# Optimization experiments

Hardware: AMD Instinct MI355X
Metric: run time of the kernel (lower is better)

The kernel has to match this reference:

```python
import jax, jax.numpy as jnp
import numpy as np

B, S, D, H, F = 4, 2048, 1024, 16, 4096
BS = 64               # sparse attention block size
DH = D // H           # head dim
EPS = 1e-5


def _layer_norm(x, g, b):
    m = jnp.mean(x, axis=-1, keepdims=True)
    v = jnp.mean(jnp.square(x - m), axis=-1, keepdims=True)
    return (x - m) * jax.lax.rsqrt(v + EPS) * g + b


def setup_inputs() -> dict:
    key = jax.random.key(0)
    ks = jax.random.split(key, 12)
    sc = 0.02
    return {
        "hidden_states": jax.random.normal(ks[0], (B, S, D), dtype=jnp.float32),
        "ln1_g": jnp.ones((D,), jnp.float32), "ln1_b": jnp.zeros((D,), jnp.float32),
        "ln2_g": jnp.ones((D,), jnp.float32), "ln2_b": jnp.zeros((D,), jnp.float32),
        "wq": jax.random.normal(ks[1], (D, D), jnp.float32) * sc, "bq": jnp.zeros((D,), jnp.float32),
        "wk": jax.random.normal(ks[2], (D, D), jnp.float32) * sc, "bk": jnp.zeros((D,), jnp.float32),
        "wv": jax.random.normal(ks[3], (D, D), jnp.float32) * sc, "bv": jnp.zeros((D,), jnp.float32),
        "wo": jax.random.normal(ks[4], (D, D), jnp.float32) * sc, "bo": jnp.zeros((D,), jnp.float32),
        "w1": jax.random.normal(ks[5], (D, F), jnp.float32) * sc, "b1": jnp.zeros((F,), jnp.float32),
        "w2": jax.random.normal(ks[6], (F, D), jnp.float32) * sc, "b2": jnp.zeros((D,), jnp.float32),
    }


def _heads(x, w, b):
    # [B,S,D] -> [B,H,S/BS,BS,DH] block layout
    y = (x @ w + b).reshape(B, S, H, DH).transpose(0, 2, 1, 3)
    return y.reshape(B, H, S // BS, BS, DH)


def _block_attention(x, wq, bq, wk, bk, wv, bv, wo, bo):
    q = _heads(x, wq, bq)
    k = _heads(x, wk, bk)
    v = _heads(x, wv, bv)
    scores = jnp.einsum("bhnqd,bhnkd->bhnqk", q, k) / jnp.sqrt(jnp.float32(DH))
    w = jax.nn.softmax(scores, axis=-1)           # block-local (sparse) attention weights
    o = jnp.einsum("bhnqk,bhnkd->bhnqd", w, v)
    o = o.reshape(B, H, S, DH).transpose(0, 2, 1, 3).reshape(B, S, D)
    return o @ wo + bo, w


def reference(hidden_states, ln1_g, ln1_b, ln2_g, ln2_b,
              wq, bq, wk, bk, wv, bv, wo, bo, w1, b1, w2, b2):
    # pre-norm attention + residual
    x1 = _layer_norm(hidden_states, ln1_g, ln1_b)
    attn_out, attn_w = _block_attention(x1, wq, bq, wk, bk, wv, bv, wo, bo)
    h = hidden_states + attn_out
    # pre-norm FFN + residual (exact GELU, matching torch nn.GELU default)
    x2 = _layer_norm(h, ln2_g, ln2_b)
    ff = jax.nn.gelu(x2 @ w1 + b1, approximate=False) @ w2 + b2
    return h + ff, attn_w
```

## Files before the change

### kernel.cpp

```cpp
#include <hip/hip_runtime.h>
#include <hip/hip_bf16.h>
#include <cmath>
#include <type_traits>

using bf16 = __hip_bfloat16;
typedef __attribute__((ext_vector_type(8))) short short8;
typedef __attribute__((ext_vector_type(4))) float f32x4;

#define LDK 72

__device__ __forceinline__ float bf2f(bf16 v){ return __bfloat162float(v); }
__device__ __forceinline__ bf16 f2bf(float v){ return __float2bfloat16(v); }

__device__ __forceinline__ void ld16(const void* g, void* l) {
    __builtin_amdgcn_global_load_lds(
        (const __attribute__((address_space(1))) void*)g,
        (__attribute__((address_space(3))) void*)l, 16, 0, 0);
}

__device__ __forceinline__ float gelu_f(float x) {
    float u = 0.7978845608028654f * x * (1.0f + 0.044715f * x * x);
    float e = __expf(2.0f * u);
    float t = 1.0f - 2.0f / (e + 1.0f);
    return 0.5f * x * (1.0f + t);
}

__global__ __launch_bounds__(256) void transpose_f32_bf16(
    const float* __restrict__ in, bf16* __restrict__ out, int R, int C)
{
    __shared__ __align__(16) bf16 tile[64][72];
    const int c0 = blockIdx.x * 64, r0 = blockIdx.y * 64;
    const int t = threadIdx.x;
    const int lr = t >> 3, lc = (t & 7) * 8;
    for (int p = 0; p < 2; ++p) {
        int r = p * 32 + lr;
        const float* src = in + (size_t)(r0 + r) * C + c0 + lc;
        float4 a = *(const float4*)src;
        float4 b = *(const float4*)(src + 4);
        tile[r][lc + 0] = f2bf(a.x); tile[r][lc + 1] = f2bf(a.y);
        tile[r][lc + 2] = f2bf(a.z); tile[r][lc + 3] = f2bf(a.w);
        tile[r][lc + 4] = f2bf(b.x); tile[r][lc + 5] = f2bf(b.y);
        tile[r][lc + 6] = f2bf(b.z); tile[r][lc + 7] = f2bf(b.w);
    }
    __syncthreads();
    for (int p = 0; p < 2; ++p) {
        int r = p * 32 + lr;
        short8 v;
        for (int j = 0; j < 8; ++j) v[j] = *(const short*)&tile[lc + j][r];
        *(short8*)(out + (size_t)(c0 + r) * R + r0 + lc) = v;
    }
}

__global__ __launch_bounds__(256) void concat_bias(
    const float* __restrict__ bq, const float* __restrict__ bk,
    const float* __restrict__ bv, float* __restrict__ out)
{
    int i = blockIdx.x * 256 + threadIdx.x;
    const float* src = (i < 1024) ? bq : ((i < 2048) ? bk : bv);
    out[i] = src[i & 1023];
}

__global__ __launch_bounds__(256) void layernorm_k(
    const float* __restrict__ x, const float* __restrict__ g,
    const float* __restrict__ bta, bf16* __restrict__ out)
{
    const int row = blockIdx.x, t = threadIdx.x;
    const float* xr = x + (size_t)row * 1024;
    float v[4], s1 = 0.f, s2 = 0.f;
    for (int j = 0; j < 4; ++j) {
        float f = xr[j * 256 + t];
        v[j] = f; s1 += f; s2 += f * f;
    }
    for (int d = 1; d < 64; d <<= 1) { s1 += __shfl_xor(s1, d); s2 += __shfl_xor(s2, d); }
    __shared__ float red[2][4];
    int wave = t >> 6, lane = t & 63;
    if (lane == 0) { red[0][wave] = s1; red[1][wave] = s2; }
    __syncthreads();
    s1 = red[0][0] + red[0][1] + red[0][2] + red[0][3];
    s2 = red[1][0] + red[1][1] + red[1][2] + red[1][3];
    float mean = s1 * (1.0f / 1024.0f);
    float var  = s2 * (1.0f / 1024.0f) - mean * mean;
    float rs   = rsqrtf(var + 1e-5f);
    bf16* orow = out + (size_t)row * 1024;
    for (int j = 0; j < 4; ++j) {
        int c = j * 256 + t;
        orow[c] = f2bf((v[j] - mean) * rs * g[c] + bta[c]);
    }
}

template <int MODE, int KT>
__global__ __launch_bounds__(512, 1) void gemm256(
    const bf16* __restrict__ A, const bf16* __restrict__ Bt,
    const float* __restrict__ bias, void* __restrict__ C,
    int M, int N)
{
    __shared__ __align__(16) bf16 smem[2][2][256 * 64];
    const int m0 = blockIdx.x * 256, n0 = blockIdx.y * 256;
    const int t = threadIdx.x;
    const int wave = t >> 6, lane = t & 63, lhi = lane >> 4, llo = lane & 15;
    const int wm = (wave >> 2) * 128;
    const int wn = (wave & 3) * 64;
    const int lrow = lane >> 3, lcol = lane & 7;
    const int gsrc = (lcol ^ lrow) * 8;

    const int axb = (wave >> 2) * 128 + (wave & 3) * 8;
    const int bxb = (wave & 3) * 64 + (wave >> 2) * 16;

    const bf16* gAX0 = A  + (size_t)(m0 + lrow + axb) * KT + gsrc;
    const bf16* gAX1 = gAX0 + (size_t)32 * KT;
    const bf16* gAY0 = gAX0 + (size_t)64 * KT;
    const bf16* gAY1 = gAX0 + (size_t)96 * KT;
    const bf16* gBX0 = Bt + (size_t)(n0 + lrow + bxb) * KT + gsrc;
    const bf16* gBX1 = gBX0 + (size_t)8 * KT;
    const bf16* gBY0 = gBX0 + (size_t)32 * KT;
    const bf16* gBY1 = gBX0 + (size_t)40 * KT;

    const int swz   = llo & 7;
    const int offA0 = (wm + llo) * 64 + ((lhi ^ swz) * 8);
    const int offA1 = (wm + llo) * 64 + ((((4 + lhi)) ^ swz) * 8);
    const int offB0 = (wn + llo) * 64 + ((lhi ^ swz) * 8);
    const int offB1 = (wn + llo) * 64 + ((((4 + lhi)) ^ swz) * 8);

    f32x4 acc[8][4];
    #pragma unroll
    for (int i = 0; i < 8; ++i)
        #pragma unroll
        for (int j = 0; j < 4; ++j) acc[i][j] = (f32x4){0.f, 0.f, 0.f, 0.f};

    constexpr int T = KT / 64;
    static_assert(T % 2 == 0, "tail assumes even tile count");

#define SBR __builtin_amdgcn_sched_barrier(0)

    ld16(gAX0, &smem[0][0][axb * 64]);        ld16(gAX1, &smem[0][0][(axb + 32) * 64]);
    ld16(gBX0, &smem[0][1][bxb * 64]);        ld16(gBX1, &smem[0][1][(bxb + 8) * 64]);
    ld16(gAY0, &smem[0][0][(axb + 64) * 64]); ld16(gAY1, &smem[0][0][(axb + 96) * 64]);
    ld16(gBY0, &smem[0][1][(bxb + 32) * 64]); ld16(gBY1, &smem[0][1][(bxb + 40) * 64]);
    gAX0 += 64; gAX1 += 64; gAY0 += 64; gAY1 += 64;
    gBX0 += 64; gBX1 += 64; gBY0 += 64; gBY1 += 64;

    auto tile = [&](auto cbc) __attribute__((always_inline)) {
        constexpr int CB = decltype(cbc)::value;
        constexpr int NB = CB ^ 1;
        short8 aX[4][2], bX[2][2], aY[4][2], bY[2][2];
        ld16(gAX0, &smem[NB][0][axb * 64]);
        ld16(gAX1, &smem[NB][0][(axb + 32) * 64]);
        asm volatile("s_waitcnt vmcnt(6)" ::: "memory");
        SBR; __builtin_amdgcn_s_barrier(); SBR;
        #pragma unroll
        for (int mi = 0; mi < 4; ++mi) {
            aX[mi][0] = *(const short8*)&smem[CB][0][offA0 + mi * 1024];
            aX[mi][1] = *(const short8*)&smem[CB][0][offA1 + mi * 1024];
        }
        #pragma unroll
        for (int ni = 0; ni < 2; ++ni) {
            bX[ni][0] = *(const short8*)&smem[CB][1][offB0 + ni * 1024];
            bX[ni][1] = *(const short8*)&smem[CB][1][offB1 + ni * 1024];
        }
        __builtin_amdgcn_s_setprio(1);
        #pragma unroll
        for (int mi = 0; mi < 4; ++mi)
            #pragma unroll
            for (int ni = 0; ni < 2; ++ni)
                #pragma unroll
                for (int kk = 0; kk < 2; ++kk)
                    acc[mi][ni] = __builtin_amdgcn_mfma_f32_16x16x32_bf16(
                        aX[mi][kk], bX[ni][kk], acc[mi][ni], 0, 0, 0);
        __builtin_amdgcn_s_setprio(0);
        ld16(gBX0, &smem[NB][1][bxb * 64]);
        ld16(gBX1, &smem[NB][1][(bxb + 8) * 64]);
        asm volatile("s_waitcnt vmcnt(4)" ::: "memory");
        SBR; __builtin_amdgcn_s_barrier(); SBR;
        #pragma unroll
        for (int ni = 0; ni < 2; ++ni) {
            bY[ni][0] = *(const short8*)&smem[CB][1][offB0 + (ni + 2) * 1024];
            bY[ni][1] = *(const short8*)&smem[CB][1][offB1 + (ni + 2) * 1024];
        }
        __builtin_amdgcn_s_setprio(1);
        #pragma unroll
        for (int mi = 0; mi < 4; ++mi)
            #pragma unroll
            for (int ni = 0; ni < 2; ++ni)
                #pragma unroll
                for (int kk = 0; kk < 2; ++kk)
                    acc[mi][ni + 2] = __builtin_amdgcn_mfma_f32_16x16x32_bf16(
                        aX[mi][kk], bY[ni][kk], acc[mi][ni + 2], 0, 0, 0);
        __builtin_amdgcn_s_setprio(0);
        ld16(gAY0, &smem[NB][0][(axb + 64) * 64]);
        ld16(gAY1, &smem[NB][0][(axb + 96) * 64]);
        #pragma unroll
        for (int mi = 0; mi < 4; ++mi) {
            aY[mi][0] = *(const short8*)&smem[CB][0][offA0 + (mi + 4) * 1024];
            aY[mi][1] = *(const short8*)&smem[CB][0][offA1 + (mi + 4) * 1024];
        }
        __builtin_amdgcn_s_setprio(1);
        #pragma unroll
        for (int mi = 0; mi < 4; ++mi)
            #pragma unroll
            for (int ni = 0; ni < 2; ++ni)
                #pragma unroll
                for (int kk = 0; kk < 2; ++kk)
                    acc[mi + 4][ni] = __builtin_amdgcn_mfma_f32_16x16x32_bf16(
                        aY[mi][kk], bX[ni][kk], acc[mi + 4][ni], 0, 0, 0);
        __builtin_amdgcn_s_setprio(0);
        ld16(gBY0, &smem[NB][1][(bxb + 32) * 64]);
        ld16(gBY1, &smem[NB][1][(bxb + 40) * 64]);
        asm volatile("s_waitcnt lgkmcnt(0)" ::: "memory");
        SBR; __builtin_amdgcn_s_barrier(); SBR;
        __builtin_amdgcn_s_setprio(1);
        #pragma unroll
        for (int mi = 0; mi < 4; ++mi)
            #pragma unroll
            for (int ni = 0; ni < 2; ++ni)
                #pragma unroll
                for (int kk = 0; kk < 2; ++kk)
                    acc[mi + 4][ni + 2] = __builtin_amdgcn_mfma_f32_16x16x32_bf16(
                        aY[mi][kk], bY[ni][kk], acc[mi + 4][ni + 2], 0, 0, 0);
        __builtin_amdgcn_s_setprio(0);
        gAX0 += 64; gAX1 += 64; gAY0 += 64; gAY1 += 64;
        gBX0 += 64; gBX1 += 64; gBY0 += 64; gBY1 += 64;
    };

    for (int jp = 0; jp < (T - 2) / 2; ++jp) {
        tile(std::integral_constant<int, 0>{});
        tile(std::integral_constant<int, 1>{});
    }
    tile(std::integral_constant<int, 0>{});

    {
        short8 aX[4][2], bX[2][2], aY[4][2], bY[2][2];
        asm volatile("s_waitcnt vmcnt(4)" ::: "memory");
        SBR; __builtin_amdgcn_s_barrier(); SBR;
        #pragma unroll
        for (int mi = 0; mi < 4; ++mi) {
            aX[mi][0] = *(const short8*)&smem[1][0][offA0 + mi * 1024];
            aX[mi][1] = *(const short8*)&smem[1][0][offA1 + mi * 1024];
        }
        #pragma unroll
        for (int ni = 0; ni < 2; ++ni) {
            bX[ni][0] = *(const short8*)&smem[1][1][offB0 + ni * 1024];
            bX[ni][1] = *(const short8*)&smem[1][1][offB1 + ni * 1024];
        }
        __builtin_amdgcn_s_setprio(1);
        #pragma unroll
        for (int mi = 0; mi < 4; ++mi)
            #pragma unroll
            for (int ni = 0; ni < 2; ++ni)
                #pragma unroll
                for (int kk = 0; kk < 2; ++kk)
                    acc[mi][ni] = __builtin_amdgcn_mfma_f32_16x16x32_bf16(
                        aX[mi][kk], bX[ni][kk], acc[mi][ni], 0, 0, 0);
        __builtin_amdgcn_s_setprio(0);
        asm volatile("s_waitcnt vmcnt(0)" ::: "memory");
        SBR; __builtin_amdgcn_s_barrier(); SBR;
        #pragma unroll
        for (int ni = 0; ni < 2; ++ni) {
            bY[ni][0] = *(const short8*)&smem[1][1][offB0 + (ni + 2) * 1024];
            bY[ni][1] = *(const short8*)&smem[1][1][offB1 + (ni + 2) * 1024];
        }
        #pragma unroll
        for (int mi = 0; mi < 4; ++mi) {
            aY[mi][0] = *(const short8*)&smem[1][0][offA0 + (mi + 4) * 1024];
            aY[mi][1] = *(const short8*)&smem[1][0][offA1 + (mi + 4) * 1024];
        }
        __builtin_amdgcn_s_setprio(1);
        #pragma unroll
        for (int mi = 0; mi < 4; ++mi)
            #pragma unroll
            for (int ni = 0; ni < 2; ++ni)
                #pragma unroll
                for (int kk = 0; kk < 2; ++kk) {
                    acc[mi][ni + 2] = __builtin_amdgcn_mfma_f32_16x16x32_bf16(
                        aX[mi][kk], bY[ni][kk], acc[mi][ni + 2], 0, 0, 0);
                    acc[mi + 4][ni] = __builtin_amdgcn_mfma_f32_16x16x32_bf16(
                        aY[mi][kk], bX[ni][kk], acc[mi + 4][ni], 0, 0, 0);
                    acc[mi + 4][ni + 2] = __builtin_amdgcn_mfma_f32_16x16x32_bf16(
                        aY[mi][kk], bY[ni][kk], acc[mi + 4][ni + 2], 0, 0, 0);
                }
        __builtin_amdgcn_s_setprio(0);
    }
#undef SBR

    #pragma unroll
    for (int mi = 0; mi < 8; ++mi)
        #pragma unroll
        for (int ni = 0; ni < 4; ++ni) {
            int row = m0 + wm + mi * 16 + lhi * 4;
            int col = n0 + wn + ni * 16 + llo;
            float bcol = bias[col];
            #pragma unroll
            for (int r = 0; r < 4; ++r) {
                size_t idx = (size_t)(row + r) * N + col;
                float v = acc[mi][ni][r] + bcol;
                if (MODE == 2) ((bf16*)C)[idx] = f2bf(gelu_f(v));
                else           ((bf16*)C)[idx] = f2bf(v);
            }
        }
}

template <int MODE, int TM>
__global__ __launch_bounds__(256) void gemm_bt(
    const bf16* __restrict__ A, const bf16* __restrict__ Bt,
    const float* __restrict__ bias, const float* __restrict__ res,
    void* __restrict__ C, int M, int N, int K)
{
    constexpr int MI = TM / 32;
    __shared__ __align__(16) bf16 As[TM * 64];
    __shared__ __align__(16) bf16 Bs[128 * 64];
    const int m0 = blockIdx.x * TM, n0 = blockIdx.y * 128;
    const int t = threadIdx.x;
    const int wave = t >> 6, lane = t & 63, lhi = lane >> 4, llo = lane & 15;
    const int wm = (wave & 1) * (TM / 2), wn = (wave >> 1) * 64;
    const int lrow = lane >> 3;
    const int lcolsw = ((lane & 7) ^ lrow) * 8;

    const bf16* Ag = A  + (size_t)(m0 + lrow) * K + lcolsw;
    const bf16* Bg = Bt + (size_t)(n0 + lrow) * K + lcolsw;

    f32x4 acc[MI][4];
    for (int i = 0; i < MI; ++i)
        for (int j = 0; j < 4; ++j) acc[i][j] = (f32x4){0.f, 0.f, 0.f, 0.f};

    auto issue = [&](int k0) {
        for (int p = 0; p < TM / 32; ++p) {
            int rb = wave * (TM / 4) + p * 8;
            ld16(Ag + (size_t)rb * K + k0, &As[rb * 64]);
        }
        for (int p = 0; p < 4; ++p) {
            int rb = wave * 32 + p * 8;
            ld16(Bg + (size_t)rb * K + k0, &Bs[rb * 64]);
        }
    };
    auto compute = [&]() {
        for (int kk = 0; kk < 64; kk += 32) {
            const int gb = kk >> 3;
            short8 af[MI], bfr[4];
            for (int i = 0; i < MI; ++i) {
                int row = wm + i * 16 + llo;
                af[i] = *(const short8*)&As[row * 64 + (((gb + lhi) ^ (llo & 7)) * 8)];
            }
            for (int i = 0; i < 4; ++i) {
                int row = wn + i * 16 + llo;
                bfr[i] = *(const short8*)&Bs[row * 64 + (((gb + lhi) ^ (llo & 7)) * 8)];
            }
            for (int mi = 0; mi < MI; ++mi)
                for (int ni = 0; ni < 4; ++ni)
                    acc[mi][ni] = __builtin_amdgcn_mfma_f32_16x16x32_bf16(
                        af[mi], bfr[ni], acc[mi][ni], 0, 0, 0);
        }
    };

    issue(0);
    __syncthreads();
    for (int k0 = 0; ; ) {
        compute();
        k0 += 64;
        if (k0 >= K) break;
        __syncthreads();
        issue(k0);
        __syncthreads();
    }

    for (int mi = 0; mi < MI; ++mi)
        for (int ni = 0; ni < 4; ++ni) {
            int row = m0 + wm + mi * 16 + lhi * 4;
            int col = n0 + wn + ni * 16 + llo;
            float bcol = bias[col];
            for (int r = 0; r < 4; ++r) {
                size_t idx = (size_t)(row + r) * N + col;
                float v = acc[mi][ni][r] + bcol;
                if (MODE == 0) {
                    ((bf16*)C)[idx] = f2bf(v);
                } else if (MODE == 1) {
                    ((float*)C)[idx] = v + res[idx];
                } else if (MODE == 2) {
                    ((bf16*)C)[idx] = f2bf(gelu_f(v));
                } else {
                    ((float*)C)[idx] = v + res[idx];
                }
            }
        }
}

__global__ __launch_bounds__(256) void attn_kernel(
    const bf16* __restrict__ qkv, float* __restrict__ attw, bf16* __restrict__ o)
{
    __shared__ __align__(16) bf16 qs[64][LDK];
    __shared__ __align__(16) bf16 ks[64][LDK];
    __shared__ __align__(16) bf16 vs[64][LDK];
    const int gid = blockIdx.x;
    const int blk = gid & 31, h = (gid >> 5) & 15, b = gid >> 9;
    const int t = threadIdx.x, wave = t >> 6, lane = t & 63;
    const int lhi = lane >> 4, llo = lane & 15;
    const int srow = t >> 3, scol = (t & 7) * 8;

    for (int p = 0; p < 2; ++p) {
        int r = p * 32 + srow;
        const bf16* base = qkv + (size_t)(b * 2048 + blk * 64 + r) * 3072 + h * 64 + scol;
        *(short8*)&qs[r][scol] = *(const short8*)(base);
        *(short8*)&ks[r][scol] = *(const short8*)(base + 1024);
        *(short8*)&vs[r][scol] = *(const short8*)(base + 2048);
    }
    __syncthreads();

    f32x4 sacc[4];
    for (int j = 0; j < 4; ++j) sacc[j] = (f32x4){0.f, 0.f, 0.f, 0.f};
    for (int kk = 0; kk < 64; kk += 32) {
        short8 aq = *(const short8*)&qs[wave * 16 + llo][kk + lhi * 8];
        for (int j = 0; j < 4; ++j) {
            short8 bk = *(const short8*)&ks[j * 16 + llo][kk + lhi * 8];
            sacc[j] = __builtin_amdgcn_mfma_f32_16x16x32_bf16(aq, bk, sacc[j], 0, 0, 0);
        }
    }
    float inv[4];
    for (int r = 0; r < 4; ++r) {
        float m = -1e30f;
        for (int j = 0; j < 4; ++j) m = fmaxf(m, sacc[j][r]);
        for (int d = 1; d < 16; d <<= 1) m = fmaxf(m, __shfl_xor(m, d));
        float s = 0.f;
        for (int j = 0; j < 4; ++j) {
            float e = expf((sacc[j][r] - m) * 0.125f);
            sacc[j][r] = e; s += e;
        }
        for (int d = 1; d < 16; d <<= 1) s += __shfl_xor(s, d);
        inv[r] = 1.0f / s;
    }
    __syncthreads();
    const size_t wbase = (size_t)gid * 4096;
    for (int j = 0; j < 4; ++j)
        for (int r = 0; r < 4; ++r) {
            int row = wave * 16 + lhi * 4 + r, col = j * 16 + llo;
            float pw = sacc[j][r] * inv[r];
            qs[row][col] = f2bf(pw);
            attw[wbase + row * 64 + col] = pw;
        }
    __syncthreads();

    f32x4 oacc[4];
    for (int nt = 0; nt < 4; ++nt) oacc[nt] = (f32x4){0.f, 0.f, 0.f, 0.f};
    for (int kk = 0; kk < 64; kk += 32) {
        short8 aw = *(const short8*)&qs[wave * 16 + llo][kk + lhi * 8];
        for (int nt = 0; nt < 4; ++nt) {
            short8 bv;
            for (int jj = 0; jj < 8; ++jj)
                bv[jj] = *(const short*)&vs[kk + lhi * 8 + jj][nt * 16 + llo];
            oacc[nt] = __builtin_amdgcn_mfma_f32_16x16x32_bf16(aw, bv, oacc[nt], 0, 0, 0);
        }
    }
    for (int nt = 0; nt < 4; ++nt)
        for (int r = 0; r < 4; ++r) {
            int row = wave * 16 + lhi * 4 + r, col = nt * 16 + llo;
            o[(size_t)(b * 2048 + blk * 64 + row) * 1024 + h * 64 + col] = f2bf(oacc[nt][r]);
        }
}

extern "C" void kernel_launch(void* const* d_in, const int* in_sizes, int n_in,
                              void* d_out, int out_size, void* d_ws, size_t ws_size,
                              hipStream_t stream)
{
    const float* hidden = (const float*)d_in[0];
    const float* ln1_g  = (const float*)d_in[1];
    const float* ln1_b  = (const float*)d_in[2];
    const float* ln2_g  = (const float*)d_in[3];
    const float* ln2_b  = (const float*)d_in[4];
    const float* wq = (const float*)d_in[5];  const float* bq = (const float*)d_in[6];
    const float* wk = (const float*)d_in[7];  const float* bk = (const float*)d_in[8];
    const float* wv = (const float*)d_in[9];  const float* bv = (const float*)d_in[10];
    const float* wo = (const float*)d_in[11]; const float* bo = (const float*)d_in[12];
    const float* w1 = (const float*)d_in[13]; const float* b1 = (const float*)d_in[14];
    const float* w2 = (const float*)d_in[15]; const float* b2 = (const float*)d_in[16];

    char* ws = (char*)d_ws;
    const size_t MB = 1u << 20;
    bf16*  wqkvT   = (bf16*)(ws +  0 * MB);
    bf16*  woT     = (bf16*)(ws +  6 * MB);
    bf16*  w1T     = (bf16*)(ws +  8 * MB);
    bf16*  w2T     = (bf16*)(ws + 16 * MB);
    float* biasQKV = (float*)(ws + 24 * MB);
    bf16*  x       = (bf16*)(ws + 25 * MB);
    bf16*  qkv     = (bf16*)(ws + 41 * MB);
    float* hbuf    = (float*)(ws + 41 * MB);
    bf16*  ffc     = (bf16*)(ws + 73 * MB);
    bf16*  obuf    = (bf16*)(ws + 89 * MB);

    float* out0 = (float*)d_out;
    float* attw = (float*)d_out + (size_t)8192 * 1024;

    transpose_f32_bf16<<<dim3(16, 16), 256, 0, stream>>>(wq, wqkvT,                 1024, 1024);
    transpose_f32_bf16<<<dim3(16, 16), 256, 0, stream>>>(wk, wqkvT + 1024 * 1024,   1024, 1024);
    transpose_f32_bf16<<<dim3(16, 16), 256, 0, stream>>>(wv, wqkvT + 2*1024*1024,   1024, 1024);
    transpose_f32_bf16<<<dim3(16, 16), 256, 0, stream>>>(wo, woT, 1024, 1024);
    transpose_f32_bf16<<<dim3(64, 16), 256, 0, stream>>>(w1, w1T, 1024, 4096);
    transpose_f32_bf16<<<dim3(16, 64), 256, 0, stream>>>(w2, w2T, 4096, 1024);
    concat_bias<<<12, 256, 0, stream>>>(bq, bk, bv, biasQKV);

    layernorm_k<<<8192, 256, 0, stream>>>(hidden, ln1_g, ln1_b, x);

    gemm256<0, 1024><<<dim3(32, 12), 512, 0, stream>>>(x, wqkvT, biasQKV, qkv,
                                                       8192, 3072);

    attn_kernel<<<2048, 256, 0, stream>>>(qkv, attw, obuf);

    gemm_bt<1, 128><<<dim3(64, 8), 256, 0, stream>>>(obuf, woT, bo, hidden, hbuf,
                                                     8192, 1024, 1024);

    layernorm_k<<<8192, 256, 0, stream>>>(hbuf, ln2_g, ln2_b, x);

    gemm256<2, 1024><<<dim3(32, 16), 512, 0, stream>>>(x, w1T, b1, ffc,
                                                       8192, 4096);

    gemm_bt<3, 128><<<dim3(64, 8), 256, 0, stream>>>(ffc, w2T, b2, hbuf, out0,
                                                     8192, 1024, 4096);
}
```

Measured before the change: 418.6 us.

## Merge weight transposes into one launch and rework GEMM barrier schedule

```diff
diff --git a/kernel.cpp b/kernel.cpp
--- a/kernel.cpp
+++ b/kernel.cpp
@@ -25,11 +25,34 @@
     return 0.5f * x * (1.0f + t);
 }
 
-__global__ __launch_bounds__(256) void transpose_f32_bf16(
-    const float* __restrict__ in, bf16* __restrict__ out, int R, int C)
-{
+__global__ __launch_bounds__(256) void transpose_all(
+    const float* __restrict__ wq, const float* __restrict__ wk,
+    const float* __restrict__ wv, const float* __restrict__ wo,
+    const float* __restrict__ w1, const float* __restrict__ w2,
+    bf16* __restrict__ wqkvT, bf16* __restrict__ woT,
+    bf16* __restrict__ w1T, bf16* __restrict__ w2T)
+{
+    const int id = blockIdx.x;
+    const float* in; bf16* out; int R, C, lbx, lby;
+    if (id < 1024) {
+        int lid = id & 255;
+        lbx = lid & 15; lby = lid >> 4; R = 1024; C = 1024;
+        if (id < 256)      { in = wq; out = wqkvT; }
+        else if (id < 512) { in = wk; out = wqkvT + 1024 * 1024; }
+        else if (id < 768) { in = wv; out = wqkvT + 2 * 1024 * 1024; }
+        else               { in = wo; out = woT; }
+    } else if (id < 2048) {
+        int lid = id - 1024;
+        lbx = lid & 63; lby = lid >> 6; R = 1024; C = 4096;
+        in = w1; out = w1T;
+    } else {
+        int lid = id - 2048;
+        lbx = lid & 15; lby = lid >> 4; R = 4096; C = 1024;
+        in = w2; out = w2T;
+    }
+
     __shared__ __align__(16) bf16 tile[64][72];
-    const int c0 = blockIdx.x * 64, r0 = blockIdx.y * 64;
+    const int c0 = lbx * 64, r0 = lby * 64;
     const int t = threadIdx.x;
     const int lr = t >> 3, lc = (t & 7) * 8;
     for (int p = 0; p < 2; ++p) {
@@ -130,7 +153,8 @@
     constexpr int T = KT / 64;
     static_assert(T % 2 == 0, "tail assumes even tile count");
 
-#define SBR __builtin_amdgcn_sched_barrier(0)
+#define SB0 __builtin_amdgcn_sched_barrier(0)
+#define SBV __builtin_amdgcn_sched_barrier(0x38F)
 
     ld16(gAX0, &smem[0][0][axb * 64]);        ld16(gAX1, &smem[0][0][(axb + 32) * 64]);
     ld16(gBX0, &smem[0][1][bxb * 64]);        ld16(gBX1, &smem[0][1][(bxb + 8) * 64]);
@@ -145,8 +169,9 @@
         short8 aX[4][2], bX[2][2], aY[4][2], bY[2][2];
         ld16(gAX0, &smem[NB][0][axb * 64]);
         ld16(gAX1, &smem[NB][0][(axb + 32) * 64]);
-        asm volatile("s_waitcnt vmcnt(6)" ::: "memory");
-        SBR; __builtin_amdgcn_s_barrier(); SBR;
+        SBV;
+        asm volatile("s_waitcnt vmcnt(2)" ::: "memory");
+        SB0; __builtin_amdgcn_s_barrier(); SB0;
         #pragma unroll
         for (int mi = 0; mi < 4; ++mi) {
             aX[mi][0] = *(const short8*)&smem[CB][0][offA0 + mi * 1024];
@@ -169,8 +194,7 @@
         __builtin_amdgcn_s_setprio(0);
         ld16(gBX0, &smem[NB][1][bxb * 64]);
         ld16(gBX1, &smem[NB][1][(bxb + 8) * 64]);
-        asm volatile("s_waitcnt vmcnt(4)" ::: "memory");
-        SBR; __builtin_amdgcn_s_barrier(); SBR;
+        SBV;
         #pragma unroll
         for (int ni = 0; ni < 2; ++ni) {
             bY[ni][0] = *(const short8*)&smem[CB][1][offB0 + (ni + 2) * 1024];
@@ -188,6 +212,7 @@
         __builtin_amdgcn_s_setprio(0);
         ld16(gAY0, &smem[NB][0][(axb + 64) * 64]);
         ld16(gAY1, &smem[NB][0][(axb + 96) * 64]);
+        SBV;
         #pragma unroll
         for (int mi = 0; mi < 4; ++mi) {
             aY[mi][0] = *(const short8*)&smem[CB][0][offA0 + (mi + 4) * 1024];
@@ -205,8 +230,7 @@
         __builtin_amdgcn_s_setprio(0);
         ld16(gBY0, &smem[NB][1][(bxb + 32) * 64]);
         ld16(gBY1, &smem[NB][1][(bxb + 40) * 64]);
-        asm volatile("s_waitcnt lgkmcnt(0)" ::: "memory");
-        SBR; __builtin_amdgcn_s_barrier(); SBR;
+        SBV;
         __builtin_amdgcn_s_setprio(1);
         #pragma unroll
         for (int mi = 0; mi < 4; ++mi)
@@ -217,6 +241,8 @@
                     acc[mi + 4][ni + 2] = __builtin_amdgcn_mfma_f32_16x16x32_bf16(
                         aY[mi][kk], bY[ni][kk], acc[mi + 4][ni + 2], 0, 0, 0);
         __builtin_amdgcn_s_setprio(0);
+        asm volatile("s_waitcnt lgkmcnt(0)" ::: "memory");
+        SB0; __builtin_amdgcn_s_barrier(); SB0;
         gAX0 += 64; gAX1 += 64; gAY0 += 64; gAY1 += 64;
         gBX0 += 64; gBX1 += 64; gBY0 += 64; gBY1 += 64;
     };
@@ -229,8 +255,8 @@
 
     {
         short8 aX[4][2], bX[2][2], aY[4][2], bY[2][2];
-        asm volatile("s_waitcnt vmcnt(4)" ::: "memory");
-        SBR; __builtin_amdgcn_s_barrier(); SBR;
+        asm volatile("s_waitcnt vmcnt(0)" ::: "memory");
+        SB0; __builtin_amdgcn_s_barrier(); SB0;
         #pragma unroll
         for (int mi = 0; mi < 4; ++mi) {
             aX[mi][0] = *(const short8*)&smem[1][0][offA0 + mi * 1024];
@@ -241,18 +267,6 @@
             bX[ni][0] = *(const short8*)&smem[1][1][offB0 + ni * 1024];
             bX[ni][1] = *(const short8*)&smem[1][1][offB1 + ni * 1024];
         }
-        __builtin_amdgcn_s_setprio(1);
-        #pragma unroll
-        for (int mi = 0; mi < 4; ++mi)
-            #pragma unroll
-            for (int ni = 0; ni < 2; ++ni)
-                #pragma unroll
-                for (int kk = 0; kk < 2; ++kk)
-                    acc[mi][ni] = __builtin_amdgcn_mfma_f32_16x16x32_bf16(
-                        aX[mi][kk], bX[ni][kk], acc[mi][ni], 0, 0, 0);
-        __builtin_amdgcn_s_setprio(0);
-        asm volatile("s_waitcnt vmcnt(0)" ::: "memory");
-        SBR; __builtin_amdgcn_s_barrier(); SBR;
         #pragma unroll
         for (int ni = 0; ni < 2; ++ni) {
             bY[ni][0] = *(const short8*)&smem[1][1][offB0 + (ni + 2) * 1024];
@@ -270,6 +284,8 @@
             for (int ni = 0; ni < 2; ++ni)
                 #pragma unroll
                 for (int kk = 0; kk < 2; ++kk) {
+                    acc[mi][ni] = __builtin_amdgcn_mfma_f32_16x16x32_bf16(
+                        aX[mi][kk], bX[ni][kk], acc[mi][ni], 0, 0, 0);
                     acc[mi][ni + 2] = __builtin_amdgcn_mfma_f32_16x16x32_bf16(
                         aX[mi][kk], bY[ni][kk], acc[mi][ni + 2], 0, 0, 0);
                     acc[mi + 4][ni] = __builtin_amdgcn_mfma_f32_16x16x32_bf16(
@@ -279,7 +295,8 @@
                 }
         __builtin_amdgcn_s_setprio(0);
     }
-#undef SBR
+#undef SB0
+#undef SBV
 
     #pragma unroll
     for (int mi = 0; mi < 8; ++mi)
@@ -486,12 +503,8 @@
     float* out0 = (float*)d_out;
     float* attw = (float*)d_out + (size_t)8192 * 1024;
 
-    transpose_f32_bf16<<<dim3(16, 16), 256, 0, stream>>>(wq, wqkvT,                 1024, 1024);
-    transpose_f32_bf16<<<dim3(16, 16), 256, 0, stream>>>(wk, wqkvT + 1024 * 1024,   1024, 1024);
-    transpose_f32_bf16<<<dim3(16, 16), 256, 0, stream>>>(wv, wqkvT + 2*1024*1024,   1024, 1024);
-    transpose_f32_bf16<<<dim3(16, 16), 256, 0, stream>>>(wo, woT, 1024, 1024);
-    transpose_f32_bf16<<<dim3(64, 16), 256, 0, stream>>>(w1, w1T, 1024, 4096);
-    transpose_f32_bf16<<<dim3(16, 64), 256, 0, stream>>>(w2, w2T, 4096, 1024);
+    transpose_all<<<3072, 256, 0, stream>>>(wq, wk, wv, wo, w1, w2,
+                                            wqkvT, woT, w1T, w2T);
     concat_bias<<<12, 256, 0, stream>>>(bq, bk, bv, biasQKV);
 
     layernorm_k<<<8192, 256, 0, stream>>>(hidden, ln1_g, ln1_b, x);
```

Measured after the change: 427.1 us. 2.0% more time.
